# Performance work log

Measured on AMD Instinct MI355X. Metric: run time of the kernel, lower is better.

The kernel has to match this reference:

```python
import jax, jax.numpy as jnp
import numpy as np

ALPHA = 0.2  # LeakyReLU negative slope
NEG_INF = -9e15  # matches torch's -9000000000000000.0


def setup_inputs() -> dict:
    key = jax.random.key(0)
    k1, k2, k3, k4 = jax.random.split(key, 4)
    B, T, N, F_in, D = 4, 32, 512, 128, 128
    h = jax.random.normal(k1, (B, T, N, F_in), dtype=jnp.float32)
    adj = jax.random.randint(k2, (N, N), 0, 2, dtype=jnp.int32)
    # params: W ~ Linear(in_dim, out_dim, bias=False); a ~ Linear(2*out_dim, 1, bias=False)
    W = jax.random.normal(k3, (F_in, D), dtype=jnp.float32) * 0.05
    a = jax.random.normal(k4, (2 * D,), dtype=jnp.float32) * 0.05
    return {"h": h, "adj": adj, "W": W, "a": a}


def reference(h, adj, W, a):
    # h: (B,T,N,F_in), adj: (N,N), W: (F_in,D), a: (2D,)
    D = W.shape[1]
    Wh = jnp.einsum('btnf,fd->btnd', h, W)  # (B,T,N,D)
    # a . [Wh_i ; Wh_j] == a_src . Wh_i + a_dst . Wh_j -- avoids (N,N,2D) concat
    a_src, a_dst = a[:D], a[D:]
    e_src = Wh @ a_src  # (B,T,N)
    e_dst = Wh @ a_dst  # (B,T,N)
    e = jax.nn.leaky_relu(e_src[..., :, None] + e_dst[..., None, :], ALPHA)  # (B,T,N,N)
    e = jnp.where(adj > 0, e, jnp.float32(NEG_INF))
    attention = jax.nn.softmax(e, axis=-1)  # dropout is identity at eval
    h_prime = jnp.einsum('btij,btjd->btid', attention, Wh)  # (B,T,N,D)
    return h_prime
```

## Files before the change

kernel.cpp:

```cpp
#include <hip/hip_runtime.h>
#include <math.h>

typedef __attribute__((ext_vector_type(8))) short bf16x8;
typedef __attribute__((ext_vector_type(4))) float f32x4;

#define MFMA(a, b, c) __builtin_amdgcn_mfma_f32_16x16x32_bf16(a, b, c, 0, 0, 0)

constexpr int GN = 128;
constexpr int NN = 512;
constexpr int FD = 128;
#define LRELU(x) fmaxf((x), 0.2f * (x))
#define NEG_BIG -9.0e15f

__device__ inline unsigned rne_top16(float x) {
    unsigned u = __float_as_uint(x);
    return u + 0x7fffu + ((u >> 16) & 1u);
}
__device__ inline unsigned pack_top16(unsigned e1, unsigned e0) {
    return __builtin_amdgcn_perm(e1, e0, 0x07060302u);
}
__device__ inline void gload16(const void* g, void* l) {
    __builtin_amdgcn_global_load_lds(
        (const __attribute__((address_space(1))) unsigned*)g,
        (__attribute__((address_space(3))) unsigned*)l, 16, 0, 0);
}

__global__ __launch_bounds__(256) void prep_kernel(
    const int* __restrict__ adj, const float* __restrict__ W,
    unsigned* __restrict__ mask, unsigned short* __restrict__ wsHi,
    unsigned short* __restrict__ wsLo)
{
    const int b = blockIdx.x, t = threadIdx.x;
    if (b < 32) {
        const int wi = b * 256 + t;
        const int row = wi >> 4, wo = wi & 15;
        const int* p = adj + row * NN + wo * 32;
        unsigned m = 0;
        #pragma unroll
        for (int q = 0; q < 32; q += 4) {
            int4 v = *(const int4*)&p[q];
            m |= (v.x > 0 ? 1u : 0u) << q;
            m |= (v.y > 0 ? 1u : 0u) << (q + 1);
            m |= (v.z > 0 ? 1u : 0u) << (q + 2);
            m |= (v.w > 0 ? 1u : 0u) << (q + 3);
        }
        mask[wi] = m;
    } else {
        const int base = (b - 32) * 512 + t * 2;
        #pragma unroll
        for (int q = 0; q < 2; ++q) {
            const int pos = base + q;
            const int idx = pos & 7, lane = (pos >> 3) & 63, cn = pos >> 9;
            const int kk = cn >> 3, nb = cn & 7;
            const int k = kk * 32 + ((lane >> 4) & 3) * 8 + idx;
            const int d = nb * 16 + (lane & 15);
            const float wv = W[k * FD + d];
            const unsigned u = __float_as_uint(wv);
            wsHi[pos] = (unsigned short)(u >> 16);
            wsLo[pos] = (unsigned short)(rne_top16(
                            wv - __uint_as_float(u & 0xffff0000u)) >> 16);
        }
    }
}

__global__ __launch_bounds__(256, 2) void whb_kernel(
    const float* __restrict__ h, const float* __restrict__ a,
    const unsigned short* __restrict__ wsHi, const unsigned short* __restrict__ wsLo,
    unsigned short* __restrict__ whtHi, unsigned short* __restrict__ whtLo,
    float* __restrict__ esrc, float* __restrict__ edst)
{
    __shared__ __attribute__((aligned(16))) unsigned short sW[32768];

    const int bid = blockIdx.x;
    const int xcd = bid & 7, slot = bid >> 3;
    const int g = xcd + 8 * (slot >> 2);
    const int jt = slot & 3;
    const int t = threadIdx.x, lane = t & 63, w = t >> 6;
    const int i0r = jt * 128;
    const int q8 = (lane >> 4) * 8;
    const float* hg = h + (size_t)(g * NN) * FD;

    for (int q = t; q < 2048; q += 256) {
        gload16(&wsHi[q * 8], &sW[q * 8]);
        gload16(&wsLo[q * 8], &sW[16384 + q * 8]);
    }
    __syncthreads();

    f32x4 acc[2][8];
    #pragma unroll
    for (int mt = 0; mt < 2; ++mt)
        #pragma unroll
        for (int nb = 0; nb < 8; ++nb) acc[mt][nb] = (f32x4){0.f, 0.f, 0.f, 0.f};

    #pragma unroll
    for (int kk = 0; kk < 4; ++kk) {
        bf16x8 ah[2], al[2];
        #pragma unroll
        for (int mt = 0; mt < 2; ++mt) {
            const float* src = hg + (size_t)(i0r + w * 32 + mt * 16 + (lane & 15)) * FD
                             + kk * 32 + q8;
            const float4 f0 = *(const float4*)src;
            const float4 f1 = *(const float4*)(src + 4);
            const float xs[8] = {f0.x, f0.y, f0.z, f0.w, f1.x, f1.y, f1.z, f1.w};
            union { bf16x8 v; unsigned u[4]; } H, L;
            #pragma unroll
            for (int j = 0; j < 4; ++j) {
                const unsigned e0 = __float_as_uint(xs[2 * j]);
                const unsigned e1 = __float_as_uint(xs[2 * j + 1]);
                H.u[j] = pack_top16(e1, e0);
                const unsigned l0 = rne_top16(xs[2*j]   - __uint_as_float(e0 & 0xffff0000u));
                const unsigned l1 = rne_top16(xs[2*j+1] - __uint_as_float(e1 & 0xffff0000u));
                L.u[j] = pack_top16(l1, l0);
            }
            ah[mt] = H.v; al[mt] = L.v;
        }
        #pragma unroll
        for (int nb = 0; nb < 8; ++nb) {
            const bf16x8 bh = *(const bf16x8*)&sW[((kk * 8 + nb) * 64 + lane) * 8];
            const bf16x8 bl = *(const bf16x8*)&sW[16384 + ((kk * 8 + nb) * 64 + lane) * 8];
            #pragma unroll
            for (int mt = 0; mt < 2; ++mt) {
                acc[mt][nb] = MFMA(al[mt], bh, acc[mt][nb]);
                acc[mt][nb] = MFMA(ah[mt], bl, acc[mt][nb]);
                acc[mt][nb] = MFMA(ah[mt], bh, acc[mt][nb]);
            }
        }
    }

    float av[8], bv[8];
    #pragma unroll
    for (int nb = 0; nb < 8; ++nb) {
        av[nb] = a[nb * 16 + (lane & 15)];
        bv[nb] = a[FD + nb * 16 + (lane & 15)];
    }
    #pragma unroll
    for (int mt = 0; mt < 2; ++mt)
        #pragma unroll
        for (int r = 0; r < 4; ++r) {
            float ps = 0.f, pd = 0.f;
            #pragma unroll
            for (int nb = 0; nb < 8; ++nb) {
                ps += acc[mt][nb][r] * av[nb];
                pd += acc[mt][nb][r] * bv[nb];
            }
            #pragma unroll
            for (int off = 1; off <= 8; off <<= 1) {
                ps += __shfl_xor(ps, off);
                pd += __shfl_xor(pd, off);
            }
            if ((lane & 15) == 0) {
                const int row = g * NN + i0r + w * 32 + mt * 16 + (lane >> 4) * 4 + r;
                esrc[row] = ps;
                edst[row] = pd;
            }
        }

    unsigned short* sTh = sW;
    unsigned short* sTl = sW + 8192;
    const size_t gbase = (size_t)g * 65536 + (size_t)jt * 16384;
    const int ib = 4 * ((lane >> 4) & 1);

    for (int ph = 0; ph < 2; ++ph) {
        __syncthreads();
        #pragma unroll
        for (int mt = 0; mt < 2; ++mt) {
            const int lp2 = (lane & 15) + 16 * (mt * 2 + (lane >> 5));
            #pragma unroll
            for (int nbp = 0; nbp < 4; ++nbp) {
                const int nb = ph * 4 + nbp;
                const int off = ((w * 4 + nbp) * 64 + lp2) * 8 + ib;
                const unsigned u0 = __float_as_uint(acc[mt][nb][0]);
                const unsigned u1 = __float_as_uint(acc[mt][nb][1]);
                const unsigned u2 = __float_as_uint(acc[mt][nb][2]);
                const unsigned u3 = __float_as_uint(acc[mt][nb][3]);
                *(uint2*)&sTh[off] = make_uint2(pack_top16(u1, u0), pack_top16(u3, u2));
                const unsigned l0 = rne_top16(acc[mt][nb][0] - __uint_as_float(u0 & 0xffff0000u));
                const unsigned l1 = rne_top16(acc[mt][nb][1] - __uint_as_float(u1 & 0xffff0000u));
                const unsigned l2 = rne_top16(acc[mt][nb][2] - __uint_as_float(u2 & 0xffff0000u));
                const unsigned l3 = rne_top16(acc[mt][nb][3] - __uint_as_float(u3 & 0xffff0000u));
                *(uint2*)&sTl[off] = make_uint2(pack_top16(l1, l0), pack_top16(l3, l2));
            }
        }
        __syncthreads();
        for (int q = t; q < 1024; q += 256) {
            const int qw = q >> 8, qr = q & 255;
            const size_t go = gbase + (size_t)(qw * 8 + ph * 4) * 512 + qr * 8;
            *(float4*)&whtHi[go] = *(const float4*)&sTh[q * 8];
            *(float4*)&whtLo[go] = *(const float4*)&sTl[q * 8];
        }
    }
}

__global__ __launch_bounds__(256, 4) void attn_kernel(
    const unsigned short* __restrict__ whtHi, const unsigned short* __restrict__ whtLo,
    const float* __restrict__ esrc, const float* __restrict__ edst,
    const unsigned* __restrict__ mask, float* __restrict__ out)
{
    __shared__ __attribute__((aligned(16))) float eds[NN];
    __shared__ __attribute__((aligned(16))) unsigned short cHi[8192];
    __shared__ __attribute__((aligned(16))) unsigned short cLo[8192];
    __shared__ float redS[4];

    const int bid = blockIdx.x;
    const int xcd = bid & 7, slot = bid >> 3;
    const int g = xcd + 8 * (slot >> 3);
    const int it = slot & 7;
    const int t = threadIdx.x, lane = t & 63, w = t >> 6;
    const int i0 = it * 64;
    const int q8 = (lane >> 4) * 8;

    const float e0 = edst[g * NN + t], e1 = edst[g * NN + 256 + t];
    eds[t] = e0; eds[t + 256] = e1;
    float mx = fmaxf(e0, e1);
    #pragma unroll
    for (int off = 1; off < 64; off <<= 1) mx = fmaxf(mx, __shfl_xor(mx, off));
    if (lane == 0) redS[w] = mx;

    const int rloc = w * 16 + (lane & 15);
    const float s0 = esrc[g * NN + i0 + rloc];
    unsigned mrow[16];
    *(uint4*)&mrow[0]  = *(const uint4*)&mask[(i0 + rloc) * 16];
    *(uint4*)&mrow[4]  = *(const uint4*)&mask[(i0 + rloc) * 16 + 4];
    *(uint4*)&mrow[8]  = *(const uint4*)&mask[(i0 + rloc) * 16 + 8];
    *(uint4*)&mrow[12] = *(const uint4*)&mask[(i0 + rloc) * 16 + 12];
    __syncthreads();
    const float maxE = fmaxf(fmaxf(redS[0], redS[1]), fmaxf(redS[2], redS[3]));
    const float mh = LRELU(s0 + maxE);

    f32x4 acc[8];
    #pragma unroll
    for (int nb = 0; nb < 8; ++nb) acc[nb] = (f32x4){0.f, 0.f, 0.f, 0.f};
    float lsum = 0.f;

    for (int c2 = 0; c2 < 8; ++c2) {
        __syncthreads();
        const size_t gb = (size_t)g * 65536 + (size_t)c2 * 8192;
        for (int q = t; q < 1024; q += 256) {
            gload16(&whtHi[gb + q * 8], &cHi[q * 8]);
            gload16(&whtLo[gb + q * 8], &cLo[q * 8]);
        }
        __syncthreads();
        #pragma unroll
        for (int kl = 0; kl < 2; ++kl) {
            const int kk = c2 * 2 + kl;
            const float* ep = &eds[kk * 32 + q8];
            const float4 ed0 = *(const float4*)ep;
            const float4 ed1 = *(const float4*)(ep + 4);
            const float ev[8] = {ed0.x, ed0.y, ed0.z, ed0.w, ed1.x, ed1.y, ed1.z, ed1.w};
            const unsigned mw = mrow[kk] >> q8;

            union { bf16x8 v; unsigned u[4]; } H;
            unsigned uh[8];
            #pragma unroll
            for (int i = 0; i < 8; ++i) {
                float x = s0 + ev[i];
                x = LRELU(x);
                x = ((mw >> i) & 1u) ? x : NEG_BIG;
                const float p = __expf(x - mh);
                const unsigned r = rne_top16(p);
                lsum += __uint_as_float(r & 0xffff0000u);
                uh[i] = r;
            }
            #pragma unroll
            for (int j = 0; j < 4; ++j) H.u[j] = pack_top16(uh[2*j+1], uh[2*j]);

            #pragma unroll
            for (int nb = 0; nb < 8; ++nb) {
                const bf16x8 bl = *(const bf16x8*)&cLo[((kl * 8 + nb) * 64 + lane) * 8];
                const bf16x8 bh = *(const bf16x8*)&cHi[((kl * 8 + nb) * 64 + lane) * 8];
                acc[nb] = MFMA(H.v, bl, acc[nb]);
                acc[nb] = MFMA(H.v, bh, acc[nb]);
            }
        }
    }

    lsum += __shfl_xor(lsum, 16);
    lsum += __shfl_xor(lsum, 32);

    #pragma unroll
    for (int r = 0; r < 4; ++r) {
        const int rr = (lane >> 4) * 4 + r;
        const float rl = 1.0f / __shfl(lsum, rr);
        const int row = g * NN + i0 + w * 16 + rr;
        #pragma unroll
        for (int nb = 0; nb < 8; ++nb)
            out[row * FD + nb * 16 + (lane & 15)] = acc[nb][r] * rl;
    }
}

extern "C" void kernel_launch(void* const* d_in, const int* in_sizes, int n_in,
                              void* d_out, int out_size, void* d_ws, size_t ws_size,
                              hipStream_t stream) {
    const float* h   = (const float*)d_in[0];
    const int*   adj = (const int*)d_in[1];
    const float* W   = (const float*)d_in[2];
    const float* a   = (const float*)d_in[3];
    float* out = (float*)d_out;

    unsigned short* whtHi = (unsigned short*)d_ws;
    unsigned short* whtLo = whtHi + (size_t)GN * 65536;
    float* esrc = (float*)(whtLo + (size_t)GN * 65536);
    float* edst = esrc + GN * NN;
    unsigned* mask = (unsigned*)(edst + GN * NN);
    unsigned short* wsHi = (unsigned short*)(mask + 8192);
    unsigned short* wsLo = wsHi + 16384;

    prep_kernel<<<64, 256, 0, stream>>>(adj, W, mask, wsHi, wsLo);
    whb_kernel<<<512, 256, 0, stream>>>(h, a, wsHi, wsLo, whtHi, whtLo, esrc, edst);
    attn_kernel<<<1024, 256, 0, stream>>>(whtHi, whtLo, esrc, edst, mask, out);
}
```

Baseline: 130.7 us.

## Double row tile per attention block, prefetch Wh chunks via registers, hoist h loads

The attention kernel now gives each wave two 16-row tiles (128 rows per block) and runs on half as many blocks. Each staged Wh chunk in LDS is therefore reused by twice as many MFMAs, which halves the number of times Wh is read from global memory. The global-to-LDS async loads are replaced by a register-prefetch double buffer: the next chunk is loaded into registers while the current one is computed. In the whb kernel all h loads are issued up front, before the weight staging, to overlap their latency. The cost is higher register pressure, so launch bounds drop to 2 blocks per SM, and there is less parallelism with 512 blocks.

```diff
diff --git a/kernel.cpp b/kernel.cpp
--- a/kernel.cpp
+++ b/kernel.cpp
@@ -80,6 +80,16 @@
     const int q8 = (lane >> 4) * 8;
     const float* hg = h + (size_t)(g * NN) * FD;
 
+    float4 hv[16];
+    #pragma unroll
+    for (int kk = 0; kk < 4; ++kk)
+        #pragma unroll
+        for (int mt = 0; mt < 2; ++mt) {
+            const float* src = hg + (size_t)(i0r + w * 32 + mt * 16 + (lane & 15)) * FD
+                             + kk * 32 + q8;
+            hv[(kk * 2 + mt) * 2 + 0] = *(const float4*)src;
+            hv[(kk * 2 + mt) * 2 + 1] = *(const float4*)(src + 4);
+        }
     for (int q = t; q < 2048; q += 256) {
         gload16(&wsHi[q * 8], &sW[q * 8]);
         gload16(&wsLo[q * 8], &sW[16384 + q * 8]);
@@ -97,10 +107,8 @@
         bf16x8 ah[2], al[2];
         #pragma unroll
         for (int mt = 0; mt < 2; ++mt) {
-            const float* src = hg + (size_t)(i0r + w * 32 + mt * 16 + (lane & 15)) * FD
-                             + kk * 32 + q8;
-            const float4 f0 = *(const float4*)src;
-            const float4 f1 = *(const float4*)(src + 4);
+            const float4 f0 = hv[(kk * 2 + mt) * 2 + 0];
+            const float4 f1 = hv[(kk * 2 + mt) * 2 + 1];
             const float xs[8] = {f0.x, f0.y, f0.z, f0.w, f1.x, f1.y, f1.z, f1.w};
             union { bf16x8 v; unsigned u[4]; } H, L;
             #pragma unroll
@@ -191,7 +199,7 @@
     }
 }
 
-__global__ __launch_bounds__(256, 4) void attn_kernel(
+__global__ __launch_bounds__(256, 2) void attn_kernel(
     const unsigned short* __restrict__ whtHi, const unsigned short* __restrict__ whtLo,
     const float* __restrict__ esrc, const float* __restrict__ edst,
     const unsigned* __restrict__ mask, float* __restrict__ out)
@@ -203,10 +211,10 @@
 
     const int bid = blockIdx.x;
     const int xcd = bid & 7, slot = bid >> 3;
-    const int g = xcd + 8 * (slot >> 3);
-    const int it = slot & 7;
+    const int g = xcd + 8 * (slot >> 2);
+    const int it = slot & 3;
     const int t = threadIdx.x, lane = t & 63, w = t >> 6;
-    const int i0 = it * 64;
+    const int i0 = it * 128;
     const int q8 = (lane >> 4) * 8;
 
     const float e0 = edst[g * NN + t], e1 = edst[g * NN + 256 + t];
@@ -216,30 +224,53 @@
     for (int off = 1; off < 64; off <<= 1) mx = fmaxf(mx, __shfl_xor(mx, off));
     if (lane == 0) redS[w] = mx;
 
-    const int rloc = w * 16 + (lane & 15);
-    const float s0 = esrc[g * NN + i0 + rloc];
-    unsigned mrow[16];
-    *(uint4*)&mrow[0]  = *(const uint4*)&mask[(i0 + rloc) * 16];
-    *(uint4*)&mrow[4]  = *(const uint4*)&mask[(i0 + rloc) * 16 + 4];
-    *(uint4*)&mrow[8]  = *(const uint4*)&mask[(i0 + rloc) * 16 + 8];
-    *(uint4*)&mrow[12] = *(const uint4*)&mask[(i0 + rloc) * 16 + 12];
+    const int rloc0 = w * 32 + (lane & 15);
+    const int rloc1 = rloc0 + 16;
+    const float s0 = esrc[g * NN + i0 + rloc0];
+    const float s1 = esrc[g * NN + i0 + rloc1];
+    unsigned m0[16], m1[16];
+    #pragma unroll
+    for (int q = 0; q < 4; ++q) {
+        *(uint4*)&m0[q * 4] = *(const uint4*)&mask[(i0 + rloc0) * 16 + q * 4];
+        *(uint4*)&m1[q * 4] = *(const uint4*)&mask[(i0 + rloc1) * 16 + q * 4];
+    }
     __syncthreads();
     const float maxE = fmaxf(fmaxf(redS[0], redS[1]), fmaxf(redS[2], redS[3]));
-    const float mh = LRELU(s0 + maxE);
-
-    f32x4 acc[8];
-    #pragma unroll
-    for (int nb = 0; nb < 8; ++nb) acc[nb] = (f32x4){0.f, 0.f, 0.f, 0.f};
-    float lsum = 0.f;
-
+    const float mh0 = LRELU(s0 + maxE);
+    const float mh1 = LRELU(s1 + maxE);
+
+    const size_t gbase = (size_t)g * 65536;
+    float4 pHi[4], pLo[4];
+    #pragma unroll
+    for (int i = 0; i < 4; ++i) {
+        pHi[i] = *(const float4*)&whtHi[gbase + (size_t)(t + 256 * i) * 8];
+        pLo[i] = *(const float4*)&whtLo[gbase + (size_t)(t + 256 * i) * 8];
+    }
+
+    f32x4 acc[2][8];
+    #pragma unroll
+    for (int mt = 0; mt < 2; ++mt)
+        #pragma unroll
+        for (int nb = 0; nb < 8; ++nb) acc[mt][nb] = (f32x4){0.f, 0.f, 0.f, 0.f};
+    float lsum0 = 0.f, lsum1 = 0.f;
+
+    #pragma unroll
     for (int c2 = 0; c2 < 8; ++c2) {
         __syncthreads();
-        const size_t gb = (size_t)g * 65536 + (size_t)c2 * 8192;
-        for (int q = t; q < 1024; q += 256) {
-            gload16(&whtHi[gb + q * 8], &cHi[q * 8]);
-            gload16(&whtLo[gb + q * 8], &cLo[q * 8]);
+        #pragma unroll
+        for (int i = 0; i < 4; ++i) {
+            *(float4*)&cHi[(t + 256 * i) * 8] = pHi[i];
+            *(float4*)&cLo[(t + 256 * i) * 8] = pLo[i];
         }
         __syncthreads();
+        if (c2 < 7) {
+            const size_t gb = gbase + (size_t)(c2 + 1) * 8192;
+            #pragma unroll
+            for (int i = 0; i < 4; ++i) {
+                pHi[i] = *(const float4*)&whtHi[gb + (size_t)(t + 256 * i) * 8];
+                pLo[i] = *(const float4*)&whtLo[gb + (size_t)(t + 256 * i) * 8];
+            }
+        }
         #pragma unroll
         for (int kl = 0; kl < 2; ++kl) {
             const int kk = c2 * 2 + kl;
@@ -247,44 +278,60 @@
             const float4 ed0 = *(const float4*)ep;
             const float4 ed1 = *(const float4*)(ep + 4);
             const float ev[8] = {ed0.x, ed0.y, ed0.z, ed0.w, ed1.x, ed1.y, ed1.z, ed1.w};
-            const unsigned mw = mrow[kk] >> q8;
-
-            union { bf16x8 v; unsigned u[4]; } H;
-            unsigned uh[8];
+            const unsigned mw0 = m0[kk] >> q8;
+            const unsigned mw1 = m1[kk] >> q8;
+
+            union { bf16x8 v; unsigned u[4]; } H0, H1;
+            unsigned uh0[8], uh1[8];
             #pragma unroll
             for (int i = 0; i < 8; ++i) {
                 float x = s0 + ev[i];
                 x = LRELU(x);
-                x = ((mw >> i) & 1u) ? x : NEG_BIG;
-                const float p = __expf(x - mh);
+                x = ((mw0 >> i) & 1u) ? x : NEG_BIG;
+                const float p = __expf(x - mh0);
                 const unsigned r = rne_top16(p);
-                lsum += __uint_as_float(r & 0xffff0000u);
-                uh[i] = r;
-            }
-            #pragma unroll
-            for (int j = 0; j < 4; ++j) H.u[j] = pack_top16(uh[2*j+1], uh[2*j]);
-
+                lsum0 += __uint_as_float(r & 0xffff0000u);
+                uh0[i] = r;
+                float y = s1 + ev[i];
+                y = LRELU(y);
+                y = ((mw1 >> i) & 1u) ? y : NEG_BIG;
+                const float p1 = __expf(y - mh1);
+                const unsigned r1 = rne_top16(p1);
+                lsum1 += __uint_as_float(r1 & 0xffff0000u);
+                uh1[i] = r1;
+            }
+            #pragma unroll
+            for (int j = 0; j < 4; ++j) {
+                H0.u[j] = pack_top16(uh0[2*j+1], uh0[2*j]);
+                H1.u[j] = pack_top16(uh1[2*j+1], uh1[2*j]);
+            }
             #pragma unroll
             for (int nb = 0; nb < 8; ++nb) {
                 const bf16x8 bl = *(const bf16x8*)&cLo[((kl * 8 + nb) * 64 + lane) * 8];
                 const bf16x8 bh = *(const bf16x8*)&cHi[((kl * 8 + nb) * 64 + lane) * 8];
-                acc[nb] = MFMA(H.v, bl, acc[nb]);
-                acc[nb] = MFMA(H.v, bh, acc[nb]);
-            }
-        }
-    }
-
-    lsum += __shfl_xor(lsum, 16);
-    lsum += __shfl_xor(lsum, 32);
+                acc[0][nb] = MFMA(H0.v, bl, acc[0][nb]);
+                acc[0][nb] = MFMA(H0.v, bh, acc[0][nb]);
+                acc[1][nb] = MFMA(H1.v, bl, acc[1][nb]);
+                acc[1][nb] = MFMA(H1.v, bh, acc[1][nb]);
+            }
+        }
+    }
+
+    lsum0 += __shfl_xor(lsum0, 16); lsum0 += __shfl_xor(lsum0, 32);
+    lsum1 += __shfl_xor(lsum1, 16); lsum1 += __shfl_xor(lsum1, 32);
 
     #pragma unroll
     for (int r = 0; r < 4; ++r) {
         const int rr = (lane >> 4) * 4 + r;
-        const float rl = 1.0f / __shfl(lsum, rr);
-        const int row = g * NN + i0 + w * 16 + rr;
-        #pragma unroll
-        for (int nb = 0; nb < 8; ++nb)
-            out[row * FD + nb * 16 + (lane & 15)] = acc[nb][r] * rl;
+        const float rl0 = 1.0f / __shfl(lsum0, rr);
+        const float rl1 = 1.0f / __shfl(lsum1, rr);
+        const int row0 = g * NN + i0 + w * 32 + rr;
+        const int row1 = row0 + 16;
+        #pragma unroll
+        for (int nb = 0; nb < 8; ++nb) {
+            out[row0 * FD + nb * 16 + (lane & 15)] = acc[0][nb][r] * rl0;
+            out[row1 * FD + nb * 16 + (lane & 15)] = acc[1][nb][r] * rl1;
+        }
     }
 }
 
@@ -307,5 +354,5 @@
 
     prep_kernel<<<64, 256, 0, stream>>>(adj, W, mask, wsHi, wsLo);
     whb_kernel<<<512, 256, 0, stream>>>(h, a, wsHi, wsLo, whtHi, whtLo, esrc, edst);
-    attn_kernel<<<1024, 256, 0, stream>>>(whtHi, whtLo, esrc, edst, mask, out);
-}
+    attn_kernel<<<512, 256, 0, stream>>>(whtHi, whtLo, esrc, edst, mask, out);
+}
```

After: 183.1 us. +40.0%, slower.
